# Kernel tuning notes

Hardware: AMD Instinct MI355X
Metric: run time of the kernel (lower is better)

## Reference

```python
import jax, jax.numpy as jnp
import numpy as np

# HashGrid config (from tcnn encoding_config)
L = 16            # n_levels
F = 2             # n_features_per_level
T = 1 << 19       # hashmap size per level (log2_hashmap_size=19)
BASE = 16         # base_resolution
SCALE = 1.3819    # per_level_scale
N_PTS = 1048576
HID = 64
ENC_DIM = L * F   # 32

_PRIMES = (np.uint32(1), np.uint32(2654435761), np.uint32(805459861))


def _level_res(l):
    return int(np.floor(BASE * (SCALE ** l)))


def hashgrid_encode(x01, tables):
    """x01: [N,3] in [0,1]; tables: [L, T, F]. Returns [N, L*F]."""
    # 8 corner offsets of the unit cube: [8,3]
    offsets = jnp.array([[i, j, k] for i in (0, 1) for j in (0, 1) for k in (0, 1)],
                        dtype=jnp.uint32)
    off_f = offsets.astype(x01.dtype)[None]            # [1,8,3]
    outs = []
    for l in range(L):
        res = _level_res(l)
        pos = x01 * res                                # [N,3]
        p0 = jnp.floor(pos)
        frac = pos - p0                                # [N,3]
        c = p0.astype(jnp.uint32)[:, None, :] + offsets[None]   # [N,8,3] corner coords
        # trilinear weights: prod over dims of (frac if corner bit==1 else 1-frac)
        w = jnp.prod(jnp.where(off_f == 1, frac[:, None, :], 1.0 - frac[:, None, :]),
                     axis=-1)                          # [N,8]
        if (res + 1) ** 3 <= T:
            # dense indexing: grid fits in the table
            idx = c[..., 0] + c[..., 1] * (res + 1) + c[..., 2] * ((res + 1) ** 2)
        else:
            # instant-ngp spatial hash (uint32 wraparound arithmetic)
            idx = (c[..., 0] * _PRIMES[0]) ^ (c[..., 1] * _PRIMES[1]) ^ (c[..., 2] * _PRIMES[2])
            idx = idx & np.uint32(T - 1)
        feats = tables[l][idx.astype(jnp.int32)]       # [N,8,F] irregular gather
        outs.append(jnp.sum(w[..., None] * feats, axis=1))  # [N,F]
    return jnp.concatenate(outs, axis=-1)              # [N, L*F]


def setup_inputs() -> dict:
    key = jax.random.key(0)
    k_x, k_t, k0, k1, k2 = jax.random.split(key, 5)
    x = jax.random.uniform(k_x, (N_PTS, 3), jnp.float32, -1.0, 1.0)
    # instant-ngp initializes hash features in U(-1e-4, 1e-4)
    tables = jax.random.uniform(k_t, (L, T, F), jnp.float32, -1e-4, 1e-4)
    W0 = jax.random.normal(k0, (ENC_DIM, HID), jnp.float32) * np.sqrt(2.0 / ENC_DIM)
    W1 = jax.random.normal(k1, (HID, HID), jnp.float32) * np.sqrt(2.0 / HID)
    W2 = jax.random.normal(k2, (HID, 1), jnp.float32) * np.sqrt(2.0 / HID)
    return {"x": x, "tables": tables, "W0": W0, "W1": W1, "W2": W2}


def reference(x, tables, W0, W1, W2):
    x01 = (x + 1.0) * 0.5                      # map [-1,1] -> [0,1]
    enc = hashgrid_encode(x01, tables)         # [N,32]
    # FullyFusedMLP: bias-free, ReLU hidden, linear output (clip_sdf=None)
    h = jax.nn.relu(enc @ W0)
    h = jax.nn.relu(h @ W1)
    return h @ W2                              # [N,1] SDF
```

## Files before the change

### kernel.cpp

```cpp
#include <hip/hip_runtime.h>
#include <stdint.h>


#define NLVL 16
#define TBLSZ (1u << 19)
#define HID 64
#define ENCD 32

typedef float f32x4 __attribute__((ext_vector_type(4)));
typedef float f32x2 __attribute__((ext_vector_type(2)));

__device__ constexpr int RES[NLVL] = {16, 22, 30, 42, 58, 80, 111, 153, 212, 294,
                                      406, 561, 775, 1072, 1481, 2047};

struct Corner8 {
    uint32_t i[8];
    float w[8];
};

__device__ __forceinline__ void corner_idx(int l, float x01, float y01, float z01,
                                           Corner8& c)
{
    const int res = RES[l];
    const float fres = (float)res;
    const float px = x01 * fres, py = y01 * fres, pz = z01 * fres;
    const float fx = floorf(px), fy = floorf(py), fz = floorf(pz);
    const float tx = px - fx, ty = py - fy, tz = pz - fz;
    const uint32_t cx = (uint32_t)fx, cy = (uint32_t)fy, cz = (uint32_t)fz;

    if (l < 5) {
        const uint32_t s1 = (uint32_t)(res + 1);
        const uint32_t s2 = s1 * s1;
        const uint32_t bx0 = cx, bx1 = cx + 1u;
        const uint32_t by0 = cy * s1, by1 = by0 + s1;
        const uint32_t bz0 = cz * s2, bz1 = bz0 + s2;
        c.i[0] = bx0 + by0 + bz0; c.i[1] = bx0 + by0 + bz1;
        c.i[2] = bx0 + by1 + bz0; c.i[3] = bx0 + by1 + bz1;
        c.i[4] = bx1 + by0 + bz0; c.i[5] = bx1 + by0 + bz1;
        c.i[6] = bx1 + by1 + bz0; c.i[7] = bx1 + by1 + bz1;
    } else {
        const uint32_t P1 = 2654435761u, P2 = 805459861u;
        const uint32_t M = TBLSZ - 1u;
        const uint32_t hx0 = cx, hx1 = cx + 1u;
        const uint32_t hy0 = cy * P1, hy1 = hy0 + P1;
        const uint32_t hz0 = cz * P2, hz1 = hz0 + P2;
        c.i[0] = (hx0 ^ hy0 ^ hz0) & M; c.i[1] = (hx0 ^ hy0 ^ hz1) & M;
        c.i[2] = (hx0 ^ hy1 ^ hz0) & M; c.i[3] = (hx0 ^ hy1 ^ hz1) & M;
        c.i[4] = (hx1 ^ hy0 ^ hz0) & M; c.i[5] = (hx1 ^ hy0 ^ hz1) & M;
        c.i[6] = (hx1 ^ hy1 ^ hz0) & M; c.i[7] = (hx1 ^ hy1 ^ hz1) & M;
    }

    const float wx1 = tx, wx0 = 1.0f - tx;
    const float wy1 = ty, wy0 = 1.0f - ty;
    const float wz1 = tz, wz0 = 1.0f - tz;
    const float w00 = wx0 * wy0, w01 = wx0 * wy1;
    const float w10 = wx1 * wy0, w11 = wx1 * wy1;
    c.w[0] = w00 * wz0; c.w[1] = w00 * wz1;
    c.w[2] = w01 * wz0; c.w[3] = w01 * wz1;
    c.w[4] = w10 * wz0; c.w[5] = w10 * wz1;
    c.w[6] = w11 * wz0; c.w[7] = w11 * wz1;
}

__device__ __forceinline__ void gather8(const Corner8& c, const float2* __restrict__ tab,
                                        float2 f[8])
{
    #pragma unroll
    for (int p = 0; p < 4; ++p) {
        const uint32_t i0 = c.i[p], i1 = c.i[p + 4];
        if ((i0 ^ i1) == 1u) {
            const f32x4 q = *(const f32x4*)&tab[i0 & ~1u];
            if (i0 & 1u) {
                f[p]     = make_float2(q.z, q.w);
                f[p + 4] = make_float2(q.x, q.y);
            } else {
                f[p]     = make_float2(q.x, q.y);
                f[p + 4] = make_float2(q.z, q.w);
            }
        } else {
            f[p]     = tab[i0];
            f[p + 4] = tab[i1];
        }
    }
}

__device__ __forceinline__ void wsum8(const Corner8& c, const float2* __restrict__ f,
                                      float& e0, float& e1)
{
    e0 = c.w[0] * f[0].x;
    e1 = c.w[0] * f[0].y;
    #pragma unroll
    for (int k = 1; k < 8; ++k) {
        e0 = fmaf(c.w[k], f[k].x, e0);
        e1 = fmaf(c.w[k], f[k].y, e1);
    }
}

__global__ __launch_bounds__(256)
void encode_level2(const float* __restrict__ x,
                   const float* __restrict__ tables,
                   float2* __restrict__ enc, int npts)
{
    const int l = blockIdx.y;
    const int t = blockIdx.x * 256 + threadIdx.x;
    const int n0 = 2 * t;
    if (n0 >= npts) return;
    const bool has1 = (n0 + 1) < npts;

    const float2 a = *(const float2*)&x[6 * (size_t)t + 0];
    const float2 b = *(const float2*)&x[6 * (size_t)t + 2];
    const float2 c2 = has1 ? *(const float2*)&x[6 * (size_t)t + 4] : make_float2(0.f, 0.f);

    const float xA = (a.x + 1.0f) * 0.5f;
    const float yA = (a.y + 1.0f) * 0.5f;
    const float zA = (b.x + 1.0f) * 0.5f;
    const float xB = has1 ? (b.y + 1.0f) * 0.5f : xA;
    const float yB = has1 ? (c2.x + 1.0f) * 0.5f : yA;
    const float zB = has1 ? (c2.y + 1.0f) * 0.5f : zA;

    Corner8 A, B;
    corner_idx(l, xA, yA, zA, A);
    corner_idx(l, xB, yB, zB, B);

    const float2* tab = (const float2*)tables + (size_t)l * TBLSZ;
    float2 fA[8], fB[8];
    gather8(A, tab, fA);
    gather8(B, tab, fB);

    float eA0, eA1, eB0, eB1;
    wsum8(A, fA, eA0, eA1);
    wsum8(B, fB, eB0, eB1);

    const size_t base = (size_t)l * npts + n0;
    if (has1) {
        f32x4 v = {eA0, eA1, eB0, eB1};
        __builtin_nontemporal_store(v, (f32x4*)&enc[base]);
    } else {
        f32x2 v = {eA0, eA1};
        __builtin_nontemporal_store(v, (f32x2*)&enc[base]);
    }
}

__global__ __launch_bounds__(256)
void mlp2s(const float2* __restrict__ enc,
           const float* __restrict__ W0,
           const float* __restrict__ W1,
           const float* __restrict__ W2,
           float* __restrict__ out, int npts)
{
    const int t = blockIdx.x * 256 + threadIdx.x;
    const int n0 = 2 * t;
    if (n0 >= npts) return;
    const bool has1 = (n0 + 1) < npts;

    float h1a[HID], h1b[HID];
    #pragma unroll
    for (int j = 0; j < HID; ++j) { h1a[j] = 0.0f; h1b[j] = 0.0f; }

    #pragma unroll 1
    for (int l = 0; l < NLVL; ++l) {
        f32x4 e;
        if (has1) {
            e = __builtin_nontemporal_load((const f32x4*)&enc[(size_t)l * npts + n0]);
        } else {
            const f32x2 ea = __builtin_nontemporal_load(
                (const f32x2*)&enc[(size_t)l * npts + n0]);
            e.x = ea.x; e.y = ea.y; e.z = ea.x; e.w = ea.y;
        }
        #pragma unroll
        for (int j4 = 0; j4 < HID / 4; ++j4) {
            const f32x4 w0 = *(const f32x4*)&W0[(2 * l) * HID + 4 * j4];
            const f32x4 w1 = *(const f32x4*)&W0[(2 * l + 1) * HID + 4 * j4];
            #pragma unroll
            for (int k = 0; k < 4; ++k) {
                h1a[4 * j4 + k] = fmaf(e.x, w0[k], fmaf(e.y, w1[k], h1a[4 * j4 + k]));
                h1b[4 * j4 + k] = fmaf(e.z, w0[k], fmaf(e.w, w1[k], h1b[4 * j4 + k]));
            }
        }
    }

    #pragma unroll
    for (int j = 0; j < HID; ++j) {
        h1a[j] = fmaxf(h1a[j], 0.0f);
        h1b[j] = fmaxf(h1b[j], 0.0f);
    }

    float accA = 0.0f, accB = 0.0f;
    #pragma unroll 1
    for (int jb = 0; jb < 4; ++jb) {
        float h2a[HID / 4], h2b[HID / 4];
        #pragma unroll
        for (int j = 0; j < HID / 4; ++j) { h2a[j] = 0.0f; h2b[j] = 0.0f; }

        #pragma unroll
        for (int i = 0; i < HID; ++i) {
            const float ra = h1a[i], rb = h1b[i];
            const float* wrow = &W1[i * HID + jb * (HID / 4)];
            #pragma unroll
            for (int j4 = 0; j4 < HID / 16; ++j4) {
                const f32x4 w = *(const f32x4*)&wrow[4 * j4];
                #pragma unroll
                for (int k = 0; k < 4; ++k) {
                    h2a[4 * j4 + k] = fmaf(ra, w[k], h2a[4 * j4 + k]);
                    h2b[4 * j4 + k] = fmaf(rb, w[k], h2b[4 * j4 + k]);
                }
            }
        }

        #pragma unroll
        for (int j4 = 0; j4 < HID / 16; ++j4) {
            const f32x4 w = *(const f32x4*)&W2[jb * (HID / 4) + 4 * j4];
            #pragma unroll
            for (int k = 0; k < 4; ++k) {
                accA = fmaf(fmaxf(h2a[4 * j4 + k], 0.0f), w[k], accA);
                accB = fmaf(fmaxf(h2b[4 * j4 + k], 0.0f), w[k], accB);
            }
        }
    }

    out[n0] = accA;
    if (has1) out[n0 + 1] = accB;
}

__global__ __launch_bounds__(256)
void sdf_fused(const float* __restrict__ x,
               const float* __restrict__ tables,
               const float* __restrict__ W0,
               const float* __restrict__ W1,
               const float* __restrict__ W2,
               float* __restrict__ out, int npts)
{
    __shared__ float sW0[ENCD * HID];
    __shared__ float sW1t[HID * HID];
    __shared__ float sW2[HID];

    const int tid = threadIdx.x;
    for (int idx = tid; idx < ENCD * HID; idx += 256) sW0[idx] = W0[idx];
    for (int idx = tid; idx < HID * HID; idx += 256) {
        const int j = idx >> 6, i = idx & 63;
        sW1t[idx] = W1[(i << 6) + j];
    }
    if (tid < HID) sW2[tid] = W2[tid];
    __syncthreads();

    const int n = blockIdx.x * 256 + tid;
    if (n >= npts) return;

    const float x01 = (x[3 * n + 0] + 1.0f) * 0.5f;
    const float y01 = (x[3 * n + 1] + 1.0f) * 0.5f;
    const float z01 = (x[3 * n + 2] + 1.0f) * 0.5f;

    float h1[HID];
    #pragma unroll
    for (int j = 0; j < HID; ++j) h1[j] = 0.0f;
    #pragma unroll
    for (int l = 0; l < NLVL; ++l) {
        Corner8 A;
        corner_idx(l, x01, y01, z01, A);
        const float2* tab = (const float2*)tables + (size_t)l * TBLSZ;
        float2 f[8];
        gather8(A, tab, f);
        float e0, e1;
        wsum8(A, f, e0, e1);
        const float* wr0 = &sW0[(2 * l) << 6];
        const float* wr1 = &sW0[(2 * l + 1) << 6];
        #pragma unroll
        for (int j = 0; j < HID; ++j)
            h1[j] = fmaf(e0, wr0[j], fmaf(e1, wr1[j], h1[j]));
    }
    #pragma unroll
    for (int j = 0; j < HID; ++j) h1[j] = fmaxf(h1[j], 0.0f);

    float acc = 0.0f;
    #pragma unroll
    for (int j = 0; j < HID; ++j) {
        const float* wr = &sW1t[j << 6];
        float t0 = 0.0f, t1 = 0.0f, t2 = 0.0f, t3 = 0.0f;
        #pragma unroll
        for (int i = 0; i < HID; i += 4) {
            t0 = fmaf(h1[i + 0], wr[i + 0], t0);
            t1 = fmaf(h1[i + 1], wr[i + 1], t1);
            t2 = fmaf(h1[i + 2], wr[i + 2], t2);
            t3 = fmaf(h1[i + 3], wr[i + 3], t3);
        }
        const float t = (t0 + t1) + (t2 + t3);
        acc = fmaf(fmaxf(t, 0.0f), sW2[j], acc);
    }
    out[n] = acc;
}

extern "C" void kernel_launch(void* const* d_in, const int* in_sizes, int n_in,
                              void* d_out, int out_size, void* d_ws, size_t ws_size,
                              hipStream_t stream) {
    const float* x      = (const float*)d_in[0];
    const float* tables = (const float*)d_in[1];
    const float* W0     = (const float*)d_in[2];
    const float* W1     = (const float*)d_in[3];
    const float* W2     = (const float*)d_in[4];
    float* out = (float*)d_out;

    const int npts = in_sizes[0] / 3;
    const size_t ws_needed = (size_t)NLVL * (size_t)npts * sizeof(float2);

    if (ws_size >= ws_needed) {
        float2* enc = (float2*)d_ws;
        const int npair = (npts + 1) / 2;
        dim3 grid((npair + 255) / 256, NLVL);
        encode_level2<<<grid, 256, 0, stream>>>(x, tables, enc, npts);
        mlp2s<<<(npair + 255) / 256, 256, 0, stream>>>(enc, W0, W1, W2, out, npts);
    } else {
        sdf_fused<<<(npts + 255) / 256, 256, 0, stream>>>(x, tables, W0, W1, W2, out, npts);
    }
}
```

Before: 634.8 us.

## Restructure MLP so each lane owns a hidden neuron with weights in registers

Replaces the per-thread-points MLP with a wave-cooperative scheme. Each lane holds one column of W0 and W1 in registers, and the wave walks its 64 points one at a time through LDS-staged encodings. The second-layer dot product uses an LDS broadcast of h1, and the output is a cross-lane shuffle reduction. The aim is to avoid the scalar/uniform weight reloads and the large per-thread hidden arrays of the old kernel. In exchange it adds a serial per-point loop with a six-step shuffle reduction and LDS round trips for every point.

```diff
diff --git a/kernel.cpp b/kernel.cpp
--- a/kernel.cpp
+++ b/kernel.cpp
@@ -6,6 +6,7 @@
 #define TBLSZ (1u << 19)
 #define HID 64
 #define ENCD 32
+#define WPTS 256
 
 typedef float f32x4 __attribute__((ext_vector_type(4)));
 typedef float f32x2 __attribute__((ext_vector_type(2)));
@@ -141,84 +142,83 @@
 }
 
 __global__ __launch_bounds__(256)
-void mlp2s(const float2* __restrict__ enc,
-           const float* __restrict__ W0,
-           const float* __restrict__ W1,
-           const float* __restrict__ W2,
-           float* __restrict__ out, int npts)
-{
-    const int t = blockIdx.x * 256 + threadIdx.x;
-    const int n0 = 2 * t;
-    if (n0 >= npts) return;
-    const bool has1 = (n0 + 1) < npts;
-
-    float h1a[HID], h1b[HID];
-    #pragma unroll
-    for (int j = 0; j < HID; ++j) { h1a[j] = 0.0f; h1b[j] = 0.0f; }
+void mlp_wt(const float2* __restrict__ enc,
+            const float* __restrict__ W0,
+            const float* __restrict__ W1,
+            const float* __restrict__ W2,
+            float* __restrict__ out, int npts)
+{
+    __shared__ float encT[4][64 * 34];
+    __shared__ float h1T[4][64];
+
+    const int tid  = threadIdx.x;
+    const int w    = tid >> 6;
+    const int lane = tid & 63;
+
+    float w0c[ENCD], w1c[HID];
+    #pragma unroll
+    for (int i = 0; i < ENCD; ++i) w0c[i] = W0[i * HID + lane];
+    #pragma unroll
+    for (int j = 0; j < HID; ++j) w1c[j] = W1[j * HID + lane];
+    const float w2c = W2[lane];
+
+    float* encW = encT[w];
+    float* h1W  = h1T[w];
+
+    const int64_t wave_base = ((int64_t)blockIdx.x * 4 + w) * WPTS;
 
     #pragma unroll 1
-    for (int l = 0; l < NLVL; ++l) {
-        f32x4 e;
-        if (has1) {
-            e = __builtin_nontemporal_load((const f32x4*)&enc[(size_t)l * npts + n0]);
-        } else {
-            const f32x2 ea = __builtin_nontemporal_load(
-                (const f32x2*)&enc[(size_t)l * npts + n0]);
-            e.x = ea.x; e.y = ea.y; e.z = ea.x; e.w = ea.y;
+    for (int c = 0; c < WPTS / 64; ++c) {
+        const int64_t n0 = wave_base + (int64_t)c * 64;
+        if (n0 >= npts) break;
+
+        #pragma unroll 8
+        for (int l = 0; l < NLVL; ++l) {
+            f32x2 e = {0.0f, 0.0f};
+            if (n0 + lane < npts)
+                e = __builtin_nontemporal_load(
+                        (const f32x2*)&enc[(size_t)l * npts + n0 + lane]);
+            *(f32x2*)&encW[lane * 34 + 2 * l] = e;
         }
-        #pragma unroll
-        for (int j4 = 0; j4 < HID / 4; ++j4) {
-            const f32x4 w0 = *(const f32x4*)&W0[(2 * l) * HID + 4 * j4];
-            const f32x4 w1 = *(const f32x4*)&W0[(2 * l + 1) * HID + 4 * j4];
+
+        float keep = 0.0f;
+        #pragma unroll 1
+        for (int p = 0; p < 64; ++p) {
+            const float* ep = &encW[p * 34];
+            float a0 = 0.0f, a1 = 0.0f;
             #pragma unroll
-            for (int k = 0; k < 4; ++k) {
-                h1a[4 * j4 + k] = fmaf(e.x, w0[k], fmaf(e.y, w1[k], h1a[4 * j4 + k]));
-                h1b[4 * j4 + k] = fmaf(e.z, w0[k], fmaf(e.w, w1[k], h1b[4 * j4 + k]));
+            for (int i = 0; i < ENCD; i += 4) {
+                const f32x2 u = *(const f32x2*)&ep[i];
+                const f32x2 v = *(const f32x2*)&ep[i + 2];
+                a0 = fmaf(u.x, w0c[i + 0], a0);
+                a1 = fmaf(u.y, w0c[i + 1], a1);
+                a0 = fmaf(v.x, w0c[i + 2], a0);
+                a1 = fmaf(v.y, w0c[i + 3], a1);
             }
+            h1W[lane] = fmaxf(a0 + a1, 0.0f);
+            float b0 = 0.0f, b1 = 0.0f, b2 = 0.0f, b3 = 0.0f;
+            #pragma unroll
+            for (int j = 0; j < HID; j += 4) {
+                const f32x4 h = *(const f32x4*)&h1W[j];
+                b0 = fmaf(h.x, w1c[j + 0], b0);
+                b1 = fmaf(h.y, w1c[j + 1], b1);
+                b2 = fmaf(h.z, w1c[j + 2], b2);
+                b3 = fmaf(h.w, w1c[j + 3], b3);
+            }
+            const float h2 = (b0 + b1) + (b2 + b3);
+            float t = fmaxf(h2, 0.0f) * w2c;
+            t += __shfl_xor(t, 32, 64);
+            t += __shfl_xor(t, 16, 64);
+            t += __shfl_xor(t, 8, 64);
+            t += __shfl_xor(t, 4, 64);
+            t += __shfl_xor(t, 2, 64);
+            t += __shfl_xor(t, 1, 64);
+            keep = (lane == p) ? t : keep;
         }
-    }
-
-    #pragma unroll
-    for (int j = 0; j < HID; ++j) {
-        h1a[j] = fmaxf(h1a[j], 0.0f);
-        h1b[j] = fmaxf(h1b[j], 0.0f);
-    }
-
-    float accA = 0.0f, accB = 0.0f;
-    #pragma unroll 1
-    for (int jb = 0; jb < 4; ++jb) {
-        float h2a[HID / 4], h2b[HID / 4];
-        #pragma unroll
-        for (int j = 0; j < HID / 4; ++j) { h2a[j] = 0.0f; h2b[j] = 0.0f; }
-
-        #pragma unroll
-        for (int i = 0; i < HID; ++i) {
-            const float ra = h1a[i], rb = h1b[i];
-            const float* wrow = &W1[i * HID + jb * (HID / 4)];
-            #pragma unroll
-            for (int j4 = 0; j4 < HID / 16; ++j4) {
-                const f32x4 w = *(const f32x4*)&wrow[4 * j4];
-                #pragma unroll
-                for (int k = 0; k < 4; ++k) {
-                    h2a[4 * j4 + k] = fmaf(ra, w[k], h2a[4 * j4 + k]);
-                    h2b[4 * j4 + k] = fmaf(rb, w[k], h2b[4 * j4 + k]);
-                }
-            }
-        }
-
-        #pragma unroll
-        for (int j4 = 0; j4 < HID / 16; ++j4) {
-            const f32x4 w = *(const f32x4*)&W2[jb * (HID / 4) + 4 * j4];
-            #pragma unroll
-            for (int k = 0; k < 4; ++k) {
-                accA = fmaf(fmaxf(h2a[4 * j4 + k], 0.0f), w[k], accA);
-                accB = fmaf(fmaxf(h2b[4 * j4 + k], 0.0f), w[k], accB);
-            }
-        }
-    }
-
-    out[n0] = accA;
-    if (has1) out[n0 + 1] = accB;
+
+        if (n0 + lane < npts)
+            out[n0 + lane] = keep;
+    }
 }
 
 __global__ __launch_bounds__(256)
@@ -304,9 +304,11 @@
     if (ws_size >= ws_needed) {
         float2* enc = (float2*)d_ws;
         const int npair = (npts + 1) / 2;
-        dim3 grid((npair + 255) / 256, NLVL);
-        encode_level2<<<grid, 256, 0, stream>>>(x, tables, enc, npts);
-        mlp2s<<<(npair + 255) / 256, 256, 0, stream>>>(enc, W0, W1, W2, out, npts);
+        dim3 egrid((npair + 255) / 256, NLVL);
+        encode_level2<<<egrid, 256, 0, stream>>>(x, tables, enc, npts);
+        const int pts_per_block = 4 * WPTS;
+        const int mblocks = (npts + pts_per_block - 1) / pts_per_block;
+        mlp_wt<<<mblocks, 256, 0, stream>>>(enc, W0, W1, W2, out, npts);
     } else {
         sdf_fused<<<(npts + 255) / 256, 256, 0, stream>>>(x, tables, W0, W1, W2, out, npts);
     }
```

Result: slower. 909.2 us (+43.2%).
